# Performance work log

Hardware: AMD Instinct MI355X
Metric: run time of the kernel (lower is better)

## Reference

```python
import jax, jax.numpy as jnp
import numpy as np
from math import factorial, sqrt

MUL = 128
LS = (0, 1, 2)
NODE_DIM = MUL * (1 + 3 + 5)   # 1152
N_NODES = 10000
N_EDGES = 50000
EDGE_DIM = 20

# ---------- real Wigner-3j (Clebsch-Gordan) coefficients ----------

def _su2_cg(j1, j2, j3, m1, m2, m3):
    if m1 + m2 != m3:
        return 0.0
    f = lambda n: factorial(int(n))
    pref = sqrt((2 * j3 + 1) * f(j1 + j2 - j3) * f(j1 - j2 + j3) * f(-j1 + j2 + j3) / f(j1 + j2 + j3 + 1))
    pref *= sqrt(f(j3 + m3) * f(j3 - m3) * f(j1 - m1) * f(j1 + m1) * f(j2 - m2) * f(j2 + m2))
    s = 0.0
    for k in range(int(j1 + j2 - j3) + 1):
        if min(j1 - m1 - k, j2 + m2 - k, j3 - j2 + m1 + k, j3 - j1 - m2 + k) < 0:
            continue
        s += (-1) ** k / (f(k) * f(j1 + j2 - j3 - k) * f(j1 - m1 - k) * f(j2 + m2 - k) * f(j3 - j2 + m1 + k) * f(j3 - j1 - m2 + k))
    return pref * s

def _q_real_to_complex(l):
    q = np.zeros((2 * l + 1, 2 * l + 1), dtype=np.complex128)
    for m in range(-l, 0):
        q[l + m, l - m] = 1 / np.sqrt(2)
        q[l + m, l + m] = -1j / np.sqrt(2)
    q[l, l] = 1.0
    for m in range(1, l + 1):
        q[l + m, l + m] = (-1) ** m / np.sqrt(2)
        q[l + m, l - m] = 1j * (-1) ** m / np.sqrt(2)
    return (-1j) ** l * q

def _real_w3j(l1, l2, l3):
    C = np.zeros((2 * l1 + 1, 2 * l2 + 1, 2 * l3 + 1))
    for a in range(2 * l1 + 1):
        for b in range(2 * l2 + 1):
            for c in range(2 * l3 + 1):
                C[a, b, c] = _su2_cg(l1, l2, l3, a - l1, b - l2, c - l3)
    Q1, Q2, Q3 = _q_real_to_complex(l1), _q_real_to_complex(l2), _q_real_to_complex(l3)
    T = np.einsum('abc,ai,bj,ck->ijk', C.astype(np.complex128), Q1, Q2, np.conj(Q3))
    W = T.real if np.linalg.norm(T.real) >= np.linalg.norm(T.imag) else T.imag
    return jnp.asarray(W / np.linalg.norm(W), dtype=jnp.float32)

# instructions from get_feasible_tp(irreps_in, irreps_in, irreps_hidden, 'uuu')
TP_PATHS = [(0, 0, 0), (0, 1, 1), (0, 2, 2), (1, 0, 1), (1, 1, 0), (1, 1, 2),
            (1, 2, 1), (2, 0, 2), (2, 1, 1), (2, 2, 0), (2, 2, 2)]
W3J = {p: _real_w3j(*p) for p in set(TP_PATHS)}
N_PATHS_TO = {0: 3, 1: 4, 2: 4}
PW = {l: float(np.sqrt((2 * l + 1) / N_PATHS_TO[l])) for l in LS}  # e3nn component/element norm
WEIGHT_NUMEL = len(TP_PATHS) * MUL  # 1408

# ---------- irreps helpers (e3nn layout: per-irrep [mul, 2l+1] blocks) ----------

def split_irreps(x):
    n = x.shape[0]
    s = x[:, :MUL]
    v1 = x[:, MUL:4 * MUL].reshape(n, MUL, 3)
    v2 = x[:, 4 * MUL:].reshape(n, MUL, 5)
    return s, v1, v2

def merge_irreps(s, v1, v2):
    n = s.shape[0]
    return jnp.concatenate([s, v1.reshape(n, -1), v2.reshape(n, -1)], axis=-1)

def o3_linear(x, W0, W1, W2, b0=None):
    s, v1, v2 = split_irreps(x)
    inv = 1.0 / np.sqrt(MUL)  # e3nn fan-in normalization
    s = s @ W0 * inv + (b0 if b0 is not None else 0.0)
    v1 = jnp.einsum('num,uv->nvm', v1, W1) * inv
    v2 = jnp.einsum('num,uv->nvm', v2, W2) * inv
    return merge_irreps(s, v1, v2)

def norm_gate(x, W1, b1, W2, b2):
    s, v1, v2 = split_irreps(x)
    n1 = jnp.linalg.norm(v1, axis=-1)  # [N, 128]
    n2 = jnp.linalg.norm(v2, axis=-1)
    f0 = jnp.concatenate([s, n1, n2], axis=-1)  # [N, 384]
    g = jax.nn.silu(f0 @ W1 + b1) @ W2 + b2
    return merge_irreps(g[:, :MUL], v1 * g[:, MUL:2 * MUL, None], v2 * g[:, 2 * MUL:, None])

def equiv_dot(x1, x2):
    s1, v11, v21 = split_irreps(x1)
    s2, v12, v22 = split_irreps(x2)
    d0 = s1 * s2
    d1 = jnp.sum(v11 * v12, -1) / np.sqrt(3.0)
    d2 = jnp.sum(v21 * v22, -1) / np.sqrt(5.0)
    return jnp.concatenate([d0, d1, d2], -1)  # [E, 384]

def tp_node_pair(x1, x2, weights):
    s1, v11, v21 = split_irreps(x1)
    s2, v12, v22 = split_irreps(x2)
    parts1 = [s1[:, :, None], v11, v21]
    parts2 = [s2[:, :, None], v12, v22]
    outs = {l: 0.0 for l in LS}
    for p, (l1, l2, l3) in enumerate(TP_PATHS):
        w = weights[:, p * MUL:(p + 1) * MUL]  # [E, 128]
        outs[l3] = outs[l3] + PW[l3] * jnp.einsum(
            'eui,euj,ijk,eu->euk', parts1[l1], parts2[l2], W3J[(l1, l2, l3)], w)
    return merge_irreps(outs[0][:, :, 0], outs[1], outs[2])

# ---------- inputs ----------

def setup_inputs() -> dict:
    key = jax.random.key(0)
    ks = jax.random.split(key, 30)
    lin = lambda k, fi, fo: jax.random.normal(k, (fi, fo), jnp.float32) / np.sqrt(fi)
    vec = lambda k, d: jax.random.normal(k, (d,), jnp.float32) * 0.1
    NI = 3 * MUL  # 384 = num_irreps
    return {
        'x': jax.random.normal(ks[0], (N_NODES, NODE_DIM), jnp.float32),
        'edge_attr': jax.random.uniform(ks[1], (N_EDGES, EDGE_DIM), jnp.float32),
        'edge_index': jax.random.randint(ks[2], (2, N_EDGES), 0, N_NODES, jnp.int32),
        'W_pre0': jax.random.normal(ks[3], (MUL, MUL), jnp.float32),
        'W_pre1': jax.random.normal(ks[4], (MUL, MUL), jnp.float32),
        'W_pre2': jax.random.normal(ks[5], (MUL, MUL), jnp.float32),
        'b_pre0': vec(ks[6], MUL),
        'ngpre_W1': lin(ks[7], NI, NI), 'ngpre_b1': vec(ks[8], NI),
        'ngpre_W2': lin(ks[9], NI, NI), 'ngpre_b2': vec(ks[10], NI),
        'es_W1': lin(ks[11], MUL + NI, 128), 'es_b1': vec(ks[12], 128),
        'es_W2': lin(ks[13], 128, WEIGHT_NUMEL), 'es_b2': vec(ks[14], WEIGHT_NUMEL),
        'er_W1': lin(ks[15], EDGE_DIM, 128), 'er_b1': vec(ks[16], 128),
        'er_W2': lin(ks[17], 128, WEIGHT_NUMEL), 'er_b2': vec(ks[18], WEIGHT_NUMEL),
        'ngpost_W1': lin(ks[19], NI, NI), 'ngpost_b1': vec(ks[20], NI),
        'ngpost_W2': lin(ks[21], NI, NI), 'ngpost_b2': vec(ks[22], NI),
        'W_post0': jax.random.normal(ks[23], (MUL, MUL), jnp.float32),
        'W_post1': jax.random.normal(ks[24], (MUL, MUL), jnp.float32),
        'W_post2': jax.random.normal(ks[25], (MUL, MUL), jnp.float32),
    }

def reference(x, edge_attr, edge_index,
              W_pre0, W_pre1, W_pre2, b_pre0,
              ngpre_W1, ngpre_b1, ngpre_W2, ngpre_b2,
              es_W1, es_b1, es_W2, es_b2,
              er_W1, er_b1, er_W2, er_b2,
              ngpost_W1, ngpost_b1, ngpost_W2, ngpost_b2,
              W_post0, W_post1, W_post2):
    src, dst = edge_index[0], edge_index[1]
    xs, xd = x[src], x[dst]
    dots = equiv_dot(xs, xd)[:, MUL:]  # drop 0e dots: [E, 256]
    s0 = jnp.concatenate([xs[:, :MUL], xd[:, :MUL], dots], axis=-1)  # [E, 512]
    tp_w = (jax.nn.silu(s0 @ es_W1 + es_b1) @ es_W2 + es_b2) \
         * (jax.nn.silu(edge_attr @ er_W1 + er_b1) @ er_W2 + er_b2)  # [E, 1408]
    x_prime = norm_gate(o3_linear(x, W_pre0, W_pre1, W_pre2, b_pre0),
                        ngpre_W1, ngpre_b1, ngpre_W2, ngpre_b2)
    fij = tp_node_pair(x_prime[src], x_prime[dst], tp_w)  # [E, 1152]
    fij = norm_gate(fij, ngpost_W1, ngpost_b1, ngpost_W2, ngpost_b2)
    fij = o3_linear(fij, W_post0, W_post1, W_post2)
    return fij
```

## Files before the change

### kernel.cpp

```cpp
#include <hip/hip_runtime.h>
#include <math.h>

#define NNODES 10000
#define NEDGES 50000
#define ND 1152
#define MUL 128
#define WNW 1408
#define EDIM 20

#define CK1 0.5773502691896258f
#define CK2 0.4472135954999579f
#define A2C 0.31622776601683794f
#define A0A (-0.18257418583505536f)
#define A0B 0.3651483716701107f
#define B1C 0.11952286093343936f
#define B2C 0.23904572186687873f
#define B3C 0.20701966780270626f
#define PW0 0.5773502691896258f
#define PW1 0.8660254037844386f
#define PW2 1.1180339887498949f
#define INV128 0.08838834764831845f

__device__ __forceinline__ float silu_f(float v) { return v / (1.f + expf(-v)); }

typedef short bfrag __attribute__((ext_vector_type(8)));
typedef float f32x4 __attribute__((ext_vector_type(4)));

__device__ __forceinline__ ushort f2bf(float f) {
    uint u = __float_as_uint(f);
    u += 0x7fffu + ((u >> 16) & 1u);
    return (ushort)(u >> 16);
}
__device__ __forceinline__ float bf2f(ushort h) {
    return __uint_as_float(((uint)h) << 16);
}

#define LSTR 40

template<int DUAL, int SILU, int ASRC, int OSINK>
__global__ __launch_bounds__(256) void gemmbf(
    const void* __restrict__ A1p, const void* __restrict__ A1s, int lda,
    const ushort* __restrict__ B1H, const ushort* __restrict__ B1L,
    const float* __restrict__ b1,
    const void* __restrict__ A2p, const void* __restrict__ A2s,
    const ushort* __restrict__ B2H, const ushort* __restrict__ B2L,
    const float* __restrict__ b2,
    const ushort* __restrict__ W2H, const ushort* __restrict__ W2L,
    float* __restrict__ C, ushort* __restrict__ CH, ushort* __restrict__ CL,
    int ldc, int M, int K, int Kreal,
    const float* __restrict__ xg, const int* __restrict__ ei,
    const float* __restrict__ dots)
{
    __shared__ __align__(16) ushort Ah[128 * LSTR];
    __shared__ __align__(16) ushort Al[128 * LSTR];
    __shared__ __align__(16) ushort Bh[128 * LSTR];
    __shared__ __align__(16) ushort Bl[128 * LSTR];

    const int tid = threadIdx.x;
    const int l   = tid & 63;
    const int wid = tid >> 6;
    const int wr  = (wid >> 1) << 6;
    const int wc  = (wid & 1) << 6;
    const int rowBase = blockIdx.y << 7;
    const int n0      = blockIdx.x << 7;

    const int sRow = tid >> 1;
    const int sK   = (tid & 1) << 4;
    const int bN   = tid & 127;
    const int bK   = (tid >> 7) << 4;

    const int frow = l & 15;
    const int fk   = (l >> 4) << 3;

    const int z = (ASRC == 3) ? blockIdx.z : 0;
    int zoff = 0, zstride = 1;
    if constexpr (ASRC == 3) {
        if (z == 0)      { zoff = 0;             zstride = 1; }
        else if (z < 4)  { zoff = 128 + (z - 1); zstride = 3; }
        else             { zoff = 512 + (z - 4); zstride = 5; }
    }

    f32x4 acc0[4][4], acc1[4][4];
#pragma unroll
    for (int m = 0; m < 4; ++m)
#pragma unroll
        for (int n = 0; n < 4; ++n) {
            acc0[m][n] = f32x4{0.f, 0.f, 0.f, 0.f};
            if constexpr (DUAL) acc1[m][n] = f32x4{0.f, 0.f, 0.f, 0.f};
        }

#pragma unroll
    for (int ph = 0; ph < (DUAL ? 2 : 1); ++ph) {
        const void* Ap  = (DUAL && ph) ? A2p : A1p;
        const void* Asp = (DUAL && ph) ? A2s : A1s;
        const ushort* BH = (DUAL && ph) ? B2H : B1H;
        const ushort* BL = (DUAL && ph) ? B2L : B1L;
        if constexpr (ASRC == 3) {
            if (z >= 1 && z < 4) { BH = B2H; BL = B2L; }
            else if (z >= 4)     { BH = W2H; BL = W2L; }
        }

        for (int k0 = 0; k0 < K; k0 += 32) {
            {
                int grow = rowBase + sRow;
                if constexpr (ASRC == 1) {
                    uint4 h0 = {0,0,0,0}, h1v = {0,0,0,0};
                    uint4 l0 = {0,0,0,0}, l1v = {0,0,0,0};
                    if (grow < M) {
                        const ushort* AH = ((const ushort*)Ap)  + (size_t)grow * lda + k0 + sK;
                        const ushort* AL = ((const ushort*)Asp) + (size_t)grow * lda + k0 + sK;
                        h0  = *(const uint4*)AH; h1v = *(const uint4*)(AH + 8);
                        l0  = *(const uint4*)AL; l1v = *(const uint4*)(AL + 8);
                    }
                    int base = sRow * LSTR + sK;
                    *(uint4*)&Ah[base]     = h0;  *(uint4*)&Ah[base + 8] = h1v;
                    *(uint4*)&Al[base]     = l0;  *(uint4*)&Al[base + 8] = l1v;
                } else {
                    float f[16];
                    if (grow < M) {
                        if constexpr (ASRC == 0) {
#pragma unroll
                            for (int j = 0; j < 16; ++j) {
                                int gk = k0 + sK + j;
                                f[j] = (gk < Kreal)
                                     ? ((const float*)Ap)[(size_t)grow * lda + gk] : 0.f;
                            }
                        } else if constexpr (ASRC == 2) {
                            int gk = k0 + sK;
                            const float4* p;
                            if (gk < 128)
                                p = (const float4*)&xg[(size_t)ei[grow] * ND + gk];
                            else if (gk < 256)
                                p = (const float4*)&xg[(size_t)ei[NEDGES + grow] * ND + (gk - 128)];
                            else
                                p = (const float4*)&dots[(size_t)grow * 256 + (gk - 256)];
#pragma unroll
                            for (int j = 0; j < 4; ++j) {
                                float4 v = p[j];
                                f[j*4+0] = v.x; f[j*4+1] = v.y;
                                f[j*4+2] = v.z; f[j*4+3] = v.w;
                            }
                        } else {
                            const float* p = &((const float*)Ap)[(size_t)grow * lda + zoff];
#pragma unroll
                            for (int j = 0; j < 16; ++j)
                                f[j] = p[(k0 + sK + j) * zstride];
                        }
                    } else {
#pragma unroll
                        for (int j = 0; j < 16; ++j) f[j] = 0.f;
                    }
                    int base = sRow * LSTR + sK;
#pragma unroll
                    for (int j = 0; j < 4; ++j) {
                        ushort4 hv, lv;
                        hv.x = f2bf(f[j*4+0]); lv.x = f2bf(f[j*4+0] - bf2f(hv.x));
                        hv.y = f2bf(f[j*4+1]); lv.y = f2bf(f[j*4+1] - bf2f(hv.y));
                        hv.z = f2bf(f[j*4+2]); lv.z = f2bf(f[j*4+2] - bf2f(hv.z));
                        hv.w = f2bf(f[j*4+3]); lv.w = f2bf(f[j*4+3] - bf2f(hv.w));
                        *(ushort4*)&Ah[base + j*4] = hv;
                        *(ushort4*)&Al[base + j*4] = lv;
                    }
                }
            }
            {
                size_t go = (size_t)(n0 + bN) * K + k0 + bK;
                uint4 h0 = *(const uint4*)&BH[go];
                uint4 h1v = *(const uint4*)&BH[go + 8];
                uint4 l0 = *(const uint4*)&BL[go];
                uint4 l1v = *(const uint4*)&BL[go + 8];
                int bb = bN * LSTR + bK;
                *(uint4*)&Bh[bb]     = h0;
                *(uint4*)&Bh[bb + 8] = h1v;
                *(uint4*)&Bl[bb]     = l0;
                *(uint4*)&Bl[bb + 8] = l1v;
            }
            __syncthreads();
            bfrag bhF[4], blF[4];
#pragma unroll
            for (int n = 0; n < 4; ++n) {
                int r = (wc + n * 16 + frow) * LSTR + fk;
                bhF[n] = *(const bfrag*)&Bh[r];
                blF[n] = *(const bfrag*)&Bl[r];
            }
#pragma unroll
            for (int m = 0; m < 4; ++m) {
                int r = (wr + m * 16 + frow) * LSTR + fk;
                bfrag ah = *(const bfrag*)&Ah[r];
                bfrag al = *(const bfrag*)&Al[r];
#pragma unroll
                for (int n = 0; n < 4; ++n) {
                    f32x4 a = (DUAL && ph) ? acc1[m][n] : acc0[m][n];
                    a = __builtin_amdgcn_mfma_f32_16x16x32_bf16(ah, bhF[n], a, 0, 0, 0);
                    a = __builtin_amdgcn_mfma_f32_16x16x32_bf16(ah, blF[n], a, 0, 0, 0);
                    a = __builtin_amdgcn_mfma_f32_16x16x32_bf16(al, bhF[n], a, 0, 0, 0);
                    if (DUAL && ph) acc1[m][n] = a; else acc0[m][n] = a;
                }
            }
            __syncthreads();
        }
    }

#pragma unroll
    for (int n = 0; n < 4; ++n) {
        int col = n0 + wc + n * 16 + frow;
        float bb1 = b1 ? b1[col] : 0.f;
        float bb2 = (DUAL && b2) ? b2[col] : 0.f;
#pragma unroll
        for (int m = 0; m < 4; ++m) {
            int row0 = rowBase + wr + m * 16 + ((l >> 4) << 2);
#pragma unroll
            for (int q = 0; q < 4; ++q) {
                int row = row0 + q;
                if (row >= M) continue;
                if constexpr (DUAL) {
                    float v = (acc0[m][n][q] + bb1) * (acc1[m][n][q] + bb2);
                    C[(size_t)row * ldc + col] = v;
                } else if constexpr (OSINK == 0) {
                    float v = acc0[m][n][q] + bb1;
                    if constexpr (SILU) v = silu_f(v);
                    C[(size_t)row * ldc + col] = v;
                } else if constexpr (OSINK == 1) {
                    float v = acc0[m][n][q] + bb1;
                    if constexpr (SILU) v = silu_f(v);
                    ushort h  = f2bf(v);
                    ushort lo = f2bf(v - bf2f(h));
                    CH[(size_t)row * ldc + col] = h;
                    CL[(size_t)row * ldc + col] = lo;
                } else {
                    float v = acc0[m][n][q] * INV128;
                    if (z == 0 && b1) v += b1[col];
                    C[(size_t)z * M * ldc + (size_t)row * ldc + col] = v;
                }
            }
        }
    }
}

template<int NPL, int OFF, int GOFF>
__global__ __launch_bounds__(256) void o3postbf(
    const float* __restrict__ fij, size_t FP,
    const float* __restrict__ g,
    const ushort* __restrict__ WH, const ushort* __restrict__ WL,
    float* __restrict__ out, int M)
{
    __shared__ __align__(16) ushort Ah[NPL * 32 * LSTR];
    __shared__ __align__(16) ushort Al[NPL * 32 * LSTR];
    __shared__ __align__(16) ushort Bh[128 * LSTR];
    __shared__ __align__(16) ushort Bl[128 * LSTR];

    const int tid = threadIdx.x;
    const int l   = tid & 63;
    const int wid = tid >> 6;
    const int wr  = (wid >> 1) << 4;
    const int wc  = (wid & 1) << 6;
    const int rowBase = blockIdx.x << 5;

    const int sR = tid >> 3;
    const int sK = (tid & 7) << 2;
    const int bN = tid & 127;
    const int bK = (tid >> 7) << 4;

    const int frow = l & 15;
    const int fk   = (l >> 4) << 3;

    f32x4 acc[NPL][4];
#pragma unroll
    for (int p = 0; p < NPL; ++p)
#pragma unroll
        for (int n = 0; n < 4; ++n) acc[p][n] = f32x4{0.f, 0.f, 0.f, 0.f};

    for (int k0 = 0; k0 < 128; k0 += 32) {
        int grow = rowBase + sR;
        float4 g4 = make_float4(0.f, 0.f, 0.f, 0.f);
        if (grow < M)
            g4 = *(const float4*)&g[(size_t)grow * 384 + GOFF + k0 + sK];
#pragma unroll
        for (int p = 0; p < NPL; ++p) {
            float4 v;
            if constexpr (NPL == 1) {
                v = g4;
            } else {
                float4 f4 = make_float4(0.f, 0.f, 0.f, 0.f);
                if (grow < M)
                    f4 = *(const float4*)&fij[(size_t)p * FP + (size_t)grow * 128 + k0 + sK];
                v = make_float4(f4.x * g4.x, f4.y * g4.y, f4.z * g4.z, f4.w * g4.w);
            }
            ushort4 hv, lv;
            hv.x = f2bf(v.x); lv.x = f2bf(v.x - bf2f(hv.x));
            hv.y = f2bf(v.y); lv.y = f2bf(v.y - bf2f(hv.y));
            hv.z = f2bf(v.z); lv.z = f2bf(v.z - bf2f(hv.z));
            hv.w = f2bf(v.w); lv.w = f2bf(v.w - bf2f(hv.w));
            int base = (p * 32 + sR) * LSTR + sK;
            *(ushort4*)&Ah[base] = hv;
            *(ushort4*)&Al[base] = lv;
        }
        {
            size_t go = (size_t)bN * 128 + k0 + bK;
            uint4 h0 = *(const uint4*)&WH[go];
            uint4 h1 = *(const uint4*)&WH[go + 8];
            uint4 l0 = *(const uint4*)&WL[go];
            uint4 l1 = *(const uint4*)&WL[go + 8];
            int bb = bN * LSTR + bK;
            *(uint4*)&Bh[bb]     = h0;
            *(uint4*)&Bh[bb + 8] = h1;
            *(uint4*)&Bl[bb]     = l0;
            *(uint4*)&Bl[bb + 8] = l1;
        }
        __syncthreads();
        bfrag bhF[4], blF[4];
#pragma unroll
        for (int n = 0; n < 4; ++n) {
            int r = (wc + n * 16 + frow) * LSTR + fk;
            bhF[n] = *(const bfrag*)&Bh[r];
            blF[n] = *(const bfrag*)&Bl[r];
        }
#pragma unroll
        for (int p = 0; p < NPL; ++p) {
            int r = (p * 32 + wr + frow) * LSTR + fk;
            bfrag ah = *(const bfrag*)&Ah[r];
            bfrag al = *(const bfrag*)&Al[r];
#pragma unroll
            for (int n = 0; n < 4; ++n) {
                acc[p][n] = __builtin_amdgcn_mfma_f32_16x16x32_bf16(ah, bhF[n], acc[p][n], 0, 0, 0);
                acc[p][n] = __builtin_amdgcn_mfma_f32_16x16x32_bf16(ah, blF[n], acc[p][n], 0, 0, 0);
                acc[p][n] = __builtin_amdgcn_mfma_f32_16x16x32_bf16(al, bhF[n], acc[p][n], 0, 0, 0);
            }
        }
        __syncthreads();
    }

#pragma unroll
    for (int n = 0; n < 4; ++n) {
        int col = wc + n * 16 + frow;
#pragma unroll
        for (int q = 0; q < 4; ++q) {
            int row = rowBase + wr + ((l >> 4) << 2) + q;
            if (row >= M) continue;
            float* po = &out[(size_t)row * ND + OFF + col * NPL];
#pragma unroll
            for (int p = 0; p < NPL; ++p)
                po[p] = acc[p][n][q] * INV128;
        }
    }
}

__global__ void wsplit_kernel(
    const float* __restrict__ W0,  const float* __restrict__ W1,
    const float* __restrict__ W2,  const float* __restrict__ W3,
    const float* __restrict__ W4,  const float* __restrict__ W5,
    const float* __restrict__ W6,  const float* __restrict__ W7,
    const float* __restrict__ W8,  const float* __restrict__ W9,
    const float* __restrict__ W10, const float* __restrict__ W11,
    const float* __restrict__ W12, const float* __restrict__ W13,
    ushort* __restrict__ out)
{
    int m = blockIdx.y;
    const float* W; int K, Kp, N; size_t off;
    switch (m) {
        case 0:  W = W0;  K = 128; Kp = 128; N = 1408; off = 0;       break;
        case 1:  W = W1;  K = 128; Kp = 128; N = 1408; off = 360448;  break;
        case 2:  W = W2;  K = 384; Kp = 384; N = 384;  off = 720896;  break;
        case 3:  W = W3;  K = 384; Kp = 384; N = 384;  off = 1015808; break;
        case 4:  W = W4;  K = 384; Kp = 384; N = 384;  off = 1310720; break;
        case 5:  W = W5;  K = 384; Kp = 384; N = 384;  off = 1605632; break;
        case 6:  W = W6;  K = 128; Kp = 128; N = 128;  off = 1900544; break;
        case 7:  W = W7;  K = 128; Kp = 128; N = 128;  off = 1933312; break;
        case 8:  W = W8;  K = 128; Kp = 128; N = 128;  off = 1966080; break;
        case 9:  W = W9;  K = 128; Kp = 128; N = 128;  off = 1998848; break;
        case 10: W = W10; K = 128; Kp = 128; N = 128;  off = 2031616; break;
        case 11: W = W11; K = 128; Kp = 128; N = 128;  off = 2064384; break;
        case 12: W = W12; K = 512; Kp = 512; N = 128;  off = 2097152; break;
        default: W = W13; K = 20;  Kp = 32;  N = 128;  off = 2228224; break;
    }
    int idx = blockIdx.x * 256 + threadIdx.x;
    if (idx >= Kp * N) return;
    int k = idx / N, n = idx - k * N;
    float v = (k < K) ? W[(size_t)k * N + n] : 0.f;
    ushort h  = f2bf(v);
    ushort lo = f2bf(v - bf2f(h));
    size_t KN = (size_t)Kp * N;
    out[off + (size_t)n * Kp + k]      = h;
    out[off + KN + (size_t)n * Kp + k] = lo;
}

__global__ void dots_kernel(const float* __restrict__ x, const int* __restrict__ ei,
                            float* __restrict__ dots)
{
    int idx = blockIdx.x * 256 + threadIdx.x;
    int e = idx >> 8, t = idx & 255;
    if (e >= NEDGES) return;
    const float* ps = x + (size_t)ei[e] * ND;
    const float* pd = x + (size_t)ei[NEDGES + e] * ND;
    float v;
    if (t < 128) {
        int u = 128 + t * 3;
        v = (ps[u] * pd[u] + ps[u + 1] * pd[u + 1] + ps[u + 2] * pd[u + 2]) * CK1;
    } else {
        int u = 512 + (t - 128) * 5;
        v = (ps[u] * pd[u] + ps[u + 1] * pd[u + 1] + ps[u + 2] * pd[u + 2]
             + ps[u + 3] * pd[u + 3] + ps[u + 4] * pd[u + 4]) * CK2;
    }
    dots[idx] = v;
}

__global__ void f0_kernel(const float* __restrict__ in,
                          ushort* __restrict__ f0H, ushort* __restrict__ f0L, int M)
{
    int idx = blockIdx.x * 256 + threadIdx.x;
    int r = idx / 384, t = idx - r * 384;
    if (r >= M) return;
    size_t P = (size_t)M * 128;
    const float* p = in + (size_t)r * 128;
    float v;
    if (t < 128) v = p[t];
    else if (t < 256) {
        int u = t - 128;
        float x1 = p[P + u], x2 = p[2 * P + u], x3 = p[3 * P + u];
        v = sqrtf(x1 * x1 + x2 * x2 + x3 * x3);
    } else {
        int u = t - 256;
        float x1 = p[4 * P + u], x2 = p[5 * P + u], x3 = p[6 * P + u],
              x4 = p[7 * P + u], x5 = p[8 * P + u];
        v = sqrtf(x1 * x1 + x2 * x2 + x3 * x3 + x4 * x4 + x5 * x5);
    }
    ushort h = f2bf(v);
    f0H[(size_t)r * 384 + t] = h;
    f0L[(size_t)r * 384 + t] = f2bf(v - bf2f(h));
}

__global__ void gate_kernel(float* __restrict__ xp, const float* __restrict__ g, int M)
{
    int t = blockIdx.x * 256 + threadIdx.x;
    if (t >= M * 128) return;
    int z = blockIdx.y;
    int r = t >> 7, u = t & 127;
    float* p = xp + (size_t)z * M * 128 + t;
    const float* gr = g + (size_t)r * 384;
    if (z == 0)      *p = gr[u];
    else if (z < 4)  *p *= gr[128 + u];
    else             *p *= gr[256 + u];
}

__global__ __launch_bounds__(256) void tp_kernel(
    const float* __restrict__ xp, const int* __restrict__ ei,
    const float* __restrict__ tpw, float* __restrict__ fij,
    ushort* __restrict__ f0H, ushort* __restrict__ f0L, int e0, int ec)
{
    int le = blockIdx.x * 2 + (threadIdx.x >> 7);
    int u = threadIdx.x & 127;
    if (le >= ec) return;
    int e = e0 + le;
    const size_t NP = (size_t)NNODES * 128;
    const float* ps = xp + (size_t)ei[e] * 128 + u;
    const float* pd = xp + (size_t)ei[NEDGES + e] * 128 + u;

    float ss = ps[0], sd = pd[0];
    float a0 = ps[NP],     a1 = ps[2 * NP], a2 = ps[3 * NP];
    float b0 = pd[NP],     b1 = pd[2 * NP], b2 = pd[3 * NP];
    float c0 = ps[4 * NP], c1 = ps[5 * NP], c2 = ps[6 * NP],
          c3 = ps[7 * NP], c4 = ps[8 * NP];
    float d0 = pd[4 * NP], d1 = pd[5 * NP], d2 = pd[6 * NP],
          d3 = pd[7 * NP], d4 = pd[8 * NP];

    const float* w = tpw + (size_t)le * WNW + u;
    float w0 = w[0],    w1 = w[128],  w2 = w[256],  w3 = w[384],  w4 = w[512];
    float w5 = w[640],  w6 = w[768],  w7 = w[896],  w8 = w[1024], w9 = w[1152];
    float w10 = w[1280];

    float dab = a0 * b0 + a1 * b1 + a2 * b2;
    float dcd = c0 * d0 + c1 * d1 + c2 * d2 + c3 * d3 + c4 * d4;

    float o_s = PW0 * (w0 * ss * sd + w4 * CK1 * dab + w9 * CK2 * dcd);

    float R0 = A0A * a0 * d2 + A2C * (a1 * d1 + a2 * d0 - a0 * d4);
    float R1 = A0B * a1 * d2 + A2C * (a0 * d1 + a2 * d3);
    float R2 = A0A * a2 * d2 + A2C * (a1 * d3 + a0 * d0 + a2 * d4);
    float U0 = A0A * b0 * c2 + A2C * (b1 * c1 + b2 * c0 - b0 * c4);
    float U1 = A0B * b1 * c2 + A2C * (b0 * c1 + b2 * c3);
    float U2 = A0A * b2 * c2 + A2C * (b1 * c3 + b0 * c0 + b2 * c4);
    float o1_0 = PW1 * (CK1 * (w1 * ss * b0 + w3 * a0 * sd) + w6 * R0 + w8 * U0);
    float o1_1 = PW1 * (CK1 * (w1 * ss * b1 + w3 * a1 * sd) + w6 * R1 + w8 * U1);
    float o1_2 = PW1 * (CK1 * (w1 * ss * b2 + w3 * a2 * sd) + w6 * R2 + w8 * U2);

    float S0 = A2C * (a0 * b2 + a2 * b0);
    float S1 = A2C * (a0 * b1 + a1 * b0);
    float S2 = A0A * (a0 * b0 + a2 * b2) + A0B * a1 * b1;
    float S3 = A2C * (a1 * b2 + a2 * b1);
    float S4 = A2C * (a2 * b2 - a0 * b0);
    float V0 = -B2C * (c0 * d2 + c2 * d0) + B3C * (c1 * d3 + c3 * d1);
    float V1 =  B3C * (c0 * d3 + c3 * d0) - B3C * (c1 * d4 + c4 * d1)
              + B1C * (c1 * d2 + c2 * d1);
    float V2 = -B2C * (c0 * d0 + c4 * d4) + B1C * (c1 * d1 + c3 * d3) + B2C * c2 * d2;
    float V3 =  B3C * (c0 * d1 + c1 * d0) + B3C * (c3 * d4 + c4 * d3)
              + B1C * (c2 * d3 + c3 * d2);
    float V4 = -B2C * (c2 * d4 + c4 * d2) - B3C * c1 * d1 + B3C * c3 * d3;
    float o2_0 = PW2 * (CK2 * (w2 * ss * d0 + w7 * c0 * sd) + w5 * S0 + w10 * V0);
    float o2_1 = PW2 * (CK2 * (w2 * ss * d1 + w7 * c1 * sd) + w5 * S1 + w10 * V1);
    float o2_2 = PW2 * (CK2 * (w2 * ss * d2 + w7 * c2 * sd) + w5 * S2 + w10 * V2);
    float o2_3 = PW2 * (CK2 * (w2 * ss * d3 + w7 * c3 * sd) + w5 * S3 + w10 * V3);
    float o2_4 = PW2 * (CK2 * (w2 * ss * d4 + w7 * c4 * sd) + w5 * S4 + w10 * V4);

    size_t FP = (size_t)ec * 128;
    float* po = fij + (size_t)le * 128 + u;
    po[0] = o_s;
    po[FP] = o1_0;     po[2 * FP] = o1_1; po[3 * FP] = o1_2;
    po[4 * FP] = o2_0; po[5 * FP] = o2_1; po[6 * FP] = o2_2;
    po[7 * FP] = o2_3; po[8 * FP] = o2_4;

    float n1 = sqrtf(o1_0 * o1_0 + o1_1 * o1_1 + o1_2 * o1_2);
    float n2 = sqrtf(o2_0 * o2_0 + o2_1 * o2_1 + o2_2 * o2_2
                     + o2_3 * o2_3 + o2_4 * o2_4);
    size_t fb = (size_t)le * 384;
    ushort h;
    h = f2bf(o_s); f0H[fb + u]       = h; f0L[fb + u]       = f2bf(o_s - bf2f(h));
    h = f2bf(n1);  f0H[fb + 128 + u] = h; f0L[fb + 128 + u] = f2bf(n1 - bf2f(h));
    h = f2bf(n2);  f0H[fb + 256 + u] = h; f0L[fb + 256 + u] = f2bf(n2 - bf2f(h));
}

extern "C" void kernel_launch(void* const* d_in, const int* in_sizes, int n_in,
                              void* d_out, int out_size, void* d_ws, size_t ws_size,
                              hipStream_t stream)
{
    const float* x         = (const float*)d_in[0];
    const float* edge_attr = (const float*)d_in[1];
    const int*   ei        = (const int*)  d_in[2];
    const float* W_pre0    = (const float*)d_in[3];
    const float* W_pre1    = (const float*)d_in[4];
    const float* W_pre2    = (const float*)d_in[5];
    const float* b_pre0    = (const float*)d_in[6];
    const float* ngpre_W1  = (const float*)d_in[7];
    const float* ngpre_b1  = (const float*)d_in[8];
    const float* ngpre_W2  = (const float*)d_in[9];
    const float* ngpre_b2  = (const float*)d_in[10];
    const float* es_W1     = (const float*)d_in[11];
    const float* es_b1     = (const float*)d_in[12];
    const float* es_W2     = (const float*)d_in[13];
    const float* es_b2     = (const float*)d_in[14];
    const float* er_W1     = (const float*)d_in[15];
    const float* er_b1     = (const float*)d_in[16];
    const float* er_W2     = (const float*)d_in[17];
    const float* er_b2     = (const float*)d_in[18];
    const float* ngpost_W1 = (const float*)d_in[19];
    const float* ngpost_b1 = (const float*)d_in[20];
    const float* ngpost_W2 = (const float*)d_in[21];
    const float* ngpost_b2 = (const float*)d_in[22];
    const float* W_post0   = (const float*)d_in[23];
    const float* W_post1   = (const float*)d_in[24];
    const float* W_post2   = (const float*)d_in[25];
    float* out = (float*)d_out;
    float* ws  = (float*)d_ws;

    float* xp    = ws;
    ushort* hesH = (ushort*)ws + 23040000;
    ushort* hesL = hesH + 6400000;
    ushort* herH = hesL + 6400000;
    ushort* herL = herH + 6400000;
    ushort* wsp  = herL + 6400000;
    const ushort* esW2H  = wsp;
    const ushort* esW2L  = wsp + 180224;
    const ushort* erW2H  = wsp + 360448;
    const ushort* erW2L  = wsp + 540672;
    const ushort* preW1H = wsp + 720896;
    const ushort* preW1L = wsp + 868352;
    const ushort* preW2H = wsp + 1015808;
    const ushort* preW2L = wsp + 1163264;
    const ushort* postW1H = wsp + 1310720;
    const ushort* postW1L = wsp + 1458176;
    const ushort* postW2H = wsp + 1605632;
    const ushort* postW2L = wsp + 1753088;
    const ushort* o3pW0H = wsp + 1900544;
    const ushort* o3pW0L = wsp + 1916928;
    const ushort* o3pW1H = wsp + 1933312;
    const ushort* o3pW1L = wsp + 1949696;
    const ushort* o3pW2H = wsp + 1966080;
    const ushort* o3pW2L = wsp + 1982464;
    const ushort* preL0H = wsp + 1998848;
    const ushort* preL0L = wsp + 2015232;
    const ushort* preL1H = wsp + 2031616;
    const ushort* preL1L = wsp + 2048000;
    const ushort* preL2H = wsp + 2064384;
    const ushort* preL2L = wsp + 2080768;
    const ushort* esW1H  = wsp + 2097152;
    const ushort* esW1L  = wsp + 2162688;
    const ushort* erW1H  = wsp + 2228224;
    const ushort* erW1L  = wsp + 2232320;
    float* arena = ws + 25438208;

    long ws_floats = (long)(ws_size / 4);
    long arena_f = ws_floats - 25438208L;
    long ec0 = arena_f / 2944;
    if (ec0 > NEDGES) ec0 = NEDGES;
    if (ec0 < 1) ec0 = 1;
    int NC = (int)((NEDGES + ec0 - 1) / ec0);
    int Ec = (NEDGES + NC - 1) / NC;

    float* dots = arena;

    wsplit_kernel<<<dim3(704, 14), 256, 0, stream>>>(
        es_W2, er_W2, ngpre_W1, ngpre_W2, ngpost_W1, ngpost_W2,
        W_post0, W_post1, W_post2, W_pre0, W_pre1, W_pre2,
        es_W1, er_W1, wsp);

    dots_kernel<<<NEDGES, 256, 0, stream>>>(x, ei, dots);

    dim3 gE(1, (NEDGES + 127) / 128);
    gemmbf<0, 1, 2, 1><<<gE, 256, 0, stream>>>(
        nullptr, nullptr, 0, esW1H, esW1L, es_b1,
        nullptr, nullptr, nullptr, nullptr, nullptr, nullptr, nullptr,
        nullptr, hesH, hesL, 128, NEDGES, 512, 512, x, ei, dots);
    gemmbf<0, 1, 0, 1><<<gE, 256, 0, stream>>>(
        edge_attr, nullptr, EDIM, erW1H, erW1L, er_b1,
        nullptr, nullptr, nullptr, nullptr, nullptr, nullptr, nullptr,
        nullptr, herH, herL, 128, NEDGES, 32, EDIM, nullptr, nullptr, nullptr);

    dim3 gO3p(1, (NNODES + 127) / 128, 9);
    gemmbf<0, 0, 3, 2><<<gO3p, 256, 0, stream>>>(
        x, nullptr, ND, preL0H, preL0L, b_pre0,
        nullptr, nullptr, preL1H, preL1L, nullptr, preL2H, preL2L,
        xp, nullptr, nullptr, 128, NNODES, 128, 128, nullptr, nullptr, nullptr);

    ushort* f0nH = (ushort*)arena;
    ushort* f0nL = f0nH + (size_t)NNODES * 384;
    ushort* hbH  = f0nL + (size_t)NNODES * 384;
    ushort* hbL  = hbH + (size_t)NNODES * 384;
    float*  gb   = arena + (size_t)NNODES * 384 * 2;
    f0_kernel<<<((size_t)NNODES * 384 + 255) / 256, 256, 0, stream>>>(xp, f0nH, f0nL, NNODES);
    dim3 gNGp(3, (NNODES + 127) / 128);
    gemmbf<0, 1, 1, 1><<<gNGp, 256, 0, stream>>>(
        f0nH, f0nL, 384, preW1H, preW1L, ngpre_b1,
        nullptr, nullptr, nullptr, nullptr, nullptr, nullptr, nullptr,
        nullptr, hbH, hbL, 384, NNODES, 384, 384, nullptr, nullptr, nullptr);
    gemmbf<0, 0, 1, 0><<<gNGp, 256, 0, stream>>>(
        hbH, hbL, 384, preW2H, preW2L, ngpre_b2,
        nullptr, nullptr, nullptr, nullptr, nullptr, nullptr, nullptr,
        gb, nullptr, nullptr, 384, NNODES, 384, 384, nullptr, nullptr, nullptr);
    dim3 gGp((NNODES * 128 + 255) / 256, 9);
    gate_kernel<<<gGp, 256, 0, stream>>>(xp, gb, NNODES);

    for (int c = 0; c < NC; ++c) {
        int e0 = c * Ec;
        int ec = NEDGES - e0; if (ec > Ec) ec = Ec;
        if (ec <= 0) break;

        float* tpwc  = arena;
        float* fijc  = tpwc + (size_t)Ec * 1408;
        ushort* f0pH = (ushort*)(fijc + (size_t)Ec * 1152);
        ushort* f0pL = f0pH + (size_t)Ec * 384;

        dim3 gW(11, (ec + 127) / 128);
        gemmbf<1, 0, 1, 0><<<gW, 256, 0, stream>>>(
            hesH + (size_t)e0 * 128, hesL + (size_t)e0 * 128, 128,
            esW2H, esW2L, es_b2,
            herH + (size_t)e0 * 128, herL + (size_t)e0 * 128,
            erW2H, erW2L, er_b2, nullptr, nullptr,
            tpwc, nullptr, nullptr, WNW, ec, 128, 128, nullptr, nullptr, nullptr);

        tp_kernel<<<(ec + 1) / 2, 256, 0, stream>>>(xp, ei, tpwc, fijc, f0pH, f0pL, e0, ec);

        ushort* h1H = (ushort*)tpwc;
        ushort* h1L = h1H + (size_t)Ec * 384;
        float*  gp  = tpwc + (size_t)Ec * 384;
        dim3 gNG(3, (ec + 127) / 128);
        gemmbf<0, 1, 1, 1><<<gNG, 256, 0, stream>>>(
            f0pH, f0pL, 384, postW1H, postW1L, ngpost_b1,
            nullptr, nullptr, nullptr, nullptr, nullptr, nullptr, nullptr,
            nullptr, h1H, h1L, 384, ec, 384, 384, nullptr, nullptr, nullptr);
        gemmbf<0, 0, 1, 0><<<gNG, 256, 0, stream>>>(
            h1H, h1L, 384, postW2H, postW2L, ngpost_b2,
            nullptr, nullptr, nullptr, nullptr, nullptr, nullptr, nullptr,
            gp, nullptr, nullptr, 384, ec, 384, 384, nullptr, nullptr, nullptr);

        size_t FPc = (size_t)ec * 128;
        int nb = (ec + 31) / 32;
        o3postbf<1, 0, 0><<<nb, 256, 0, stream>>>(
            nullptr, 0, gp, o3pW0H, o3pW0L, out + (size_t)e0 * ND, ec);
        o3postbf<3, 128, 128><<<nb, 256, 0, stream>>>(
            fijc + FPc, FPc, gp, o3pW1H, o3pW1L, out + (size_t)e0 * ND, ec);
        o3postbf<5, 512, 256><<<nb, 256, 0, stream>>>(
            fijc + 4 * FPc, FPc, gp, o3pW2H, o3pW2L, out + (size_t)e0 * ND, ec);
    }
}
```

Baseline: 1.486 ms.

## Load GEMM tiles directly into LDS with global_load_lds and XOR-swizzled layout

```diff
diff --git a/kernel.cpp b/kernel.cpp
--- a/kernel.cpp
+++ b/kernel.cpp
@@ -33,6 +33,12 @@
 }
 __device__ __forceinline__ float bf2f(ushort h) {
     return __uint_as_float(((uint)h) << 16);
+}
+
+__device__ __forceinline__ void gload16(const void* g, void* l) {
+    __builtin_amdgcn_global_load_lds(
+        (const __attribute__((address_space(1))) void*)g,
+        (__attribute__((address_space(3))) void*)l, 16, 0, 0);
 }
 
 #define LSTR 40
@@ -51,10 +57,10 @@
     const float* __restrict__ xg, const int* __restrict__ ei,
     const float* __restrict__ dots)
 {
-    __shared__ __align__(16) ushort Ah[128 * LSTR];
-    __shared__ __align__(16) ushort Al[128 * LSTR];
-    __shared__ __align__(16) ushort Bh[128 * LSTR];
-    __shared__ __align__(16) ushort Bl[128 * LSTR];
+    __shared__ __align__(16) ushort Ah[4096];
+    __shared__ __align__(16) ushort Al[4096];
+    __shared__ __align__(16) ushort Bh[4096];
+    __shared__ __align__(16) ushort Bl[4096];
 
     const int tid = threadIdx.x;
     const int l   = tid & 63;
@@ -63,14 +69,33 @@
     const int wc  = (wid & 1) << 6;
     const int rowBase = blockIdx.y << 7;
     const int n0      = blockIdx.x << 7;
+    const bool fullA  = (ASRC == 1) && (rowBase + 128 <= M);
+
+    const int gr0 = tid >> 2;
+    const int gj  = tid & 3;
+    const int gsw = ((2 * gj) ^ (gr0 & 6)) << 2;
+    const int ld0 = tid * 8;
+    const int ld1 = (tid + 256) * 8;
 
     const int sRow = tid >> 1;
-    const int sK   = (tid & 1) << 4;
-    const int bN   = tid & 127;
-    const int bK   = (tid >> 7) << 4;
+    const int sK16 = (tid & 1) << 4;
+    const int wj0  = sK16 >> 3;
+    const int wd0  = sRow * 32 + (((2 * wj0) ^ (sRow & 6)) << 2);
+    const int wd1  = sRow * 32 + (((2 * (wj0 + 1)) ^ (sRow & 6)) << 2);
 
     const int frow = l & 15;
     const int fk   = (l >> 4) << 3;
+    int aoff[4], boff[4];
+#pragma unroll
+    for (int m = 0; m < 4; ++m) {
+        int r = wr + m * 16 + frow;
+        aoff[m] = r * 32 + ((((fk >> 2)) ^ (r & 6)) << 2);
+    }
+#pragma unroll
+    for (int n = 0; n < 4; ++n) {
+        int r = wc + n * 16 + frow;
+        boff[n] = r * 32 + ((((fk >> 2)) ^ (r & 6)) << 2);
+    }
 
     const int z = (ASRC == 3) ? blockIdx.z : 0;
     int zoff = 0, zstride = 1;
@@ -100,94 +125,104 @@
             else if (z >= 4)     { BH = W2H; BL = W2L; }
         }
 
+        const ushort* bh0 = BH + (size_t)(n0 + gr0) * K + gsw;
+        const ushort* bh1 = BH + (size_t)(n0 + gr0 + 64) * K + gsw;
+        const ushort* bl0 = BL + (size_t)(n0 + gr0) * K + gsw;
+        const ushort* bl1 = BL + (size_t)(n0 + gr0 + 64) * K + gsw;
+        const ushort* ah0 = nullptr; const ushort* ah1 = nullptr;
+        const ushort* al0 = nullptr; const ushort* al1 = nullptr;
+        if constexpr (ASRC == 1) {
+            ah0 = (const ushort*)Ap  + (size_t)(rowBase + gr0) * lda + gsw;
+            ah1 = (const ushort*)Ap  + (size_t)(rowBase + gr0 + 64) * lda + gsw;
+            al0 = (const ushort*)Asp + (size_t)(rowBase + gr0) * lda + gsw;
+            al1 = (const ushort*)Asp + (size_t)(rowBase + gr0 + 64) * lda + gsw;
+        }
+
         for (int k0 = 0; k0 < K; k0 += 32) {
-            {
+            gload16(bh0 + k0, &Bh[ld0]);
+            gload16(bh1 + k0, &Bh[ld1]);
+            gload16(bl0 + k0, &Bl[ld0]);
+            gload16(bl1 + k0, &Bl[ld1]);
+            if (fullA) {
+                gload16(ah0 + k0, &Ah[ld0]);
+                gload16(ah1 + k0, &Ah[ld1]);
+                gload16(al0 + k0, &Al[ld0]);
+                gload16(al1 + k0, &Al[ld1]);
+            } else if constexpr (ASRC == 1) {
                 int grow = rowBase + sRow;
-                if constexpr (ASRC == 1) {
-                    uint4 h0 = {0,0,0,0}, h1v = {0,0,0,0};
-                    uint4 l0 = {0,0,0,0}, l1v = {0,0,0,0};
-                    if (grow < M) {
-                        const ushort* AH = ((const ushort*)Ap)  + (size_t)grow * lda + k0 + sK;
-                        const ushort* AL = ((const ushort*)Asp) + (size_t)grow * lda + k0 + sK;
-                        h0  = *(const uint4*)AH; h1v = *(const uint4*)(AH + 8);
-                        l0  = *(const uint4*)AL; l1v = *(const uint4*)(AL + 8);
-                    }
-                    int base = sRow * LSTR + sK;
-                    *(uint4*)&Ah[base]     = h0;  *(uint4*)&Ah[base + 8] = h1v;
-                    *(uint4*)&Al[base]     = l0;  *(uint4*)&Al[base + 8] = l1v;
-                } else {
-                    float f[16];
-                    if (grow < M) {
-                        if constexpr (ASRC == 0) {
-#pragma unroll
-                            for (int j = 0; j < 16; ++j) {
-                                int gk = k0 + sK + j;
-                                f[j] = (gk < Kreal)
-                                     ? ((const float*)Ap)[(size_t)grow * lda + gk] : 0.f;
-                            }
-                        } else if constexpr (ASRC == 2) {
-                            int gk = k0 + sK;
-                            const float4* p;
-                            if (gk < 128)
-                                p = (const float4*)&xg[(size_t)ei[grow] * ND + gk];
-                            else if (gk < 256)
-                                p = (const float4*)&xg[(size_t)ei[NEDGES + grow] * ND + (gk - 128)];
-                            else
-                                p = (const float4*)&dots[(size_t)grow * 256 + (gk - 256)];
-#pragma unroll
-                            for (int j = 0; j < 4; ++j) {
-                                float4 v = p[j];
-                                f[j*4+0] = v.x; f[j*4+1] = v.y;
-                                f[j*4+2] = v.z; f[j*4+3] = v.w;
-                            }
-                        } else {
-                            const float* p = &((const float*)Ap)[(size_t)grow * lda + zoff];
-#pragma unroll
-                            for (int j = 0; j < 16; ++j)
-                                f[j] = p[(k0 + sK + j) * zstride];
+                uint4 H0 = {0,0,0,0}, H1 = {0,0,0,0};
+                uint4 L0 = {0,0,0,0}, L1 = {0,0,0,0};
+                if (grow < M) {
+                    const ushort* AH = (const ushort*)Ap  + (size_t)grow * lda + k0 + sK16;
+                    const ushort* AL = (const ushort*)Asp + (size_t)grow * lda + k0 + sK16;
+                    H0 = *(const uint4*)AH; H1 = *(const uint4*)(AH + 8);
+                    L0 = *(const uint4*)AL; L1 = *(const uint4*)(AL + 8);
+                }
+                *(uint4*)&Ah[wd0] = H0; *(uint4*)&Ah[wd1] = H1;
+                *(uint4*)&Al[wd0] = L0; *(uint4*)&Al[wd1] = L1;
+            } else {
+                float f[16];
+                int grow = rowBase + sRow;
+                if (grow < M) {
+                    if constexpr (ASRC == 0) {
+#pragma unroll
+                        for (int j = 0; j < 16; ++j) {
+                            int gk = k0 + sK16 + j;
+                            f[j] = (gk < Kreal)
+                                 ? ((const float*)Ap)[(size_t)grow * lda + gk] : 0.f;
+                        }
+                    } else if constexpr (ASRC == 2) {
+                        int gk = k0 + sK16;
+                        const float4* p;
+                        if (gk < 128)
+                            p = (const float4*)&xg[(size_t)ei[grow] * ND + gk];
+                        else if (gk < 256)
+                            p = (const float4*)&xg[(size_t)ei[NEDGES + grow] * ND + (gk - 128)];
+                        else
+                            p = (const float4*)&dots[(size_t)grow * 256 + (gk - 256)];
+#pragma unroll
+                        for (int j = 0; j < 4; ++j) {
+                            float4 v = p[j];
+                            f[j*4+0] = v.x; f[j*4+1] = v.y;
+                            f[j*4+2] = v.z; f[j*4+3] = v.w;
                         }
                     } else {
-#pragma unroll
-                        for (int j = 0; j < 16; ++j) f[j] = 0.f;
+                        const float* p = &((const float*)Ap)[(size_t)grow * lda + zoff];
+#pragma unroll
+                        for (int j = 0; j < 16; ++j)
+                            f[j] = p[(k0 + sK16 + j) * zstride];
                     }
-                    int base = sRow * LSTR + sK;
-#pragma unroll
-                    for (int j = 0; j < 4; ++j) {
-                        ushort4 hv, lv;
-                        hv.x = f2bf(f[j*4+0]); lv.x = f2bf(f[j*4+0] - bf2f(hv.x));
-                        hv.y = f2bf(f[j*4+1]); lv.y = f2bf(f[j*4+1] - bf2f(hv.y));
-                        hv.z = f2bf(f[j*4+2]); lv.z = f2bf(f[j*4+2] - bf2f(hv.z));
-                        hv.w = f2bf(f[j*4+3]); lv.w = f2bf(f[j*4+3] - bf2f(hv.w));
-                        *(ushort4*)&Ah[base + j*4] = hv;
-                        *(ushort4*)&Al[base + j*4] = lv;
-                    }
+                } else {
+#pragma unroll
+                    for (int j = 0; j < 16; ++j) f[j] = 0.f;
                 }
-            }
-            {
-                size_t go = (size_t)(n0 + bN) * K + k0 + bK;
-                uint4 h0 = *(const uint4*)&BH[go];
-                uint4 h1v = *(const uint4*)&BH[go + 8];
-                uint4 l0 = *(const uint4*)&BL[go];
-                uint4 l1v = *(const uint4*)&BL[go + 8];
-                int bb = bN * LSTR + bK;
-                *(uint4*)&Bh[bb]     = h0;
-                *(uint4*)&Bh[bb + 8] = h1v;
-                *(uint4*)&Bl[bb]     = l0;
-                *(uint4*)&Bl[bb + 8] = l1v;
+                uint hw[8], lw[8];
+#pragma unroll
+                for (int jj = 0; jj < 8; ++jj) {
+                    ushort ha = f2bf(f[2*jj]),   hb = f2bf(f[2*jj+1]);
+                    ushort la = f2bf(f[2*jj]   - bf2f(ha));
+                    ushort lb = f2bf(f[2*jj+1] - bf2f(hb));
+                    hw[jj] = (uint)ha | ((uint)hb << 16);
+                    lw[jj] = (uint)la | ((uint)lb << 16);
+                }
+                uint4 H0 = {hw[0], hw[1], hw[2], hw[3]};
+                uint4 H1 = {hw[4], hw[5], hw[6], hw[7]};
+                uint4 L0 = {lw[0], lw[1], lw[2], lw[3]};
+                uint4 L1 = {lw[4], lw[5], lw[6], lw[7]};
+                *(uint4*)&Ah[wd0] = H0; *(uint4*)&Ah[wd1] = H1;
+                *(uint4*)&Al[wd0] = L0; *(uint4*)&Al[wd1] = L1;
             }
             __syncthreads();
             bfrag bhF[4], blF[4];
 #pragma unroll
             for (int n = 0; n < 4; ++n) {
-                int r = (wc + n * 16 + frow) * LSTR + fk;
-                bhF[n] = *(const bfrag*)&Bh[r];
-                blF[n] = *(const bfrag*)&Bl[r];
+                bhF[n] = *(const bfrag*)&Bh[boff[n]];
+                blF[n] = *(const bfrag*)&Bl[boff[n]];
             }
 #pragma unroll
             for (int m = 0; m < 4; ++m) {
-                int r = (wr + m * 16 + frow) * LSTR + fk;
-                bfrag ah = *(const bfrag*)&Ah[r];
-                bfrag al = *(const bfrag*)&Al[r];
+                bfrag ah = *(const bfrag*)&Ah[aoff[m]];
+                bfrag al = *(const bfrag*)&Al[aoff[m]];
 #pragma unroll
                 for (int n = 0; n < 4; ++n) {
                     f32x4 a = (DUAL && ph) ? acc1[m][n] : acc0[m][n];
```

Result: faster. 1.386 ms (-6.7%).
